# Optimization experiments

Hardware: AMD Instinct MI355X
Metric: run time of the kernel (lower is better)

Reference implementation:

```python
import jax, jax.numpy as jnp
import numpy as np

# FP4 E2M1 value table (codes 0..7 positive, 8..15 negative, sign in MSB)
FP4_VALUES = jnp.array([0.0, 0.5, 1.0, 1.5, 2.0, 3.0, 4.0, 6.0,
                        -0.0, -0.5, -1.0, -1.5, -2.0, -3.0, -4.0, -6.0],
                       dtype=jnp.float32)


def setup_inputs() -> dict:
    key = jax.random.key(0)
    k1, k2, k3, k4 = jax.random.split(key, 4)
    O, I = 4096, 4096
    block = 16
    x = jax.random.normal(k1, (8192, I), dtype=jnp.float32)
    # packed uint4 pairs stored as int32 bytes in [0, 256)
    weight = jax.random.randint(k2, (O, I // 2), 0, 256, dtype=jnp.int32)
    # per-block FP8-style scales (positive)
    weight_scale = jax.random.uniform(k3, (O, I // block), dtype=jnp.float32, minval=0.01, maxval=1.0)
    bias = jax.random.normal(k4, (O,), dtype=jnp.float32)
    return {"x": x, "weight": weight, "weight_scale": weight_scale,
            "bias": bias, "block_size": block}


def _dequant_nvfp4(weight, weight_scale, block_size):
    # unpack two FP4 codes per byte: high nibble is the even (first) element
    hi = (weight >> 4) & 0xF
    lo = weight & 0xF
    O = weight.shape[0]
    codes = jnp.stack([hi, lo], axis=-1).reshape(O, -1)  # [O, I]
    vals = FP4_VALUES[codes]                             # [O, I] f32
    I = vals.shape[1]
    # apply per-block scale
    w = vals.reshape(O, I // block_size, block_size) * weight_scale[:, :, None]
    return w.reshape(O, I)


def reference(x, weight, weight_scale, bias, block_size):
    w = _dequant_nvfp4(weight, weight_scale, block_size)  # [O, I]
    return jnp.einsum('ti,oi->to', x, w) + bias[None, :]
```

## Files before the change

kernel.cpp:

```cpp
#include <hip/hip_runtime.h>
#include <hip/hip_fp16.h>

typedef __attribute__((ext_vector_type(8))) _Float16 f16x8;
typedef __attribute__((ext_vector_type(4))) float f32x4;

#define M_DIM 8192
#define N_DIM 4096
#define K_DIM 4096
#define BM 256
#define BN 256
#define BK 32
#define NT (K_DIM / BK)
#define TILE_F16 ((BM + BN) * BK)

__constant__ float FP4_LUT[16] = {0.f, 0.5f, 1.f, 1.5f, 2.f, 3.f, 4.f, 6.f,
                                  -0.f, -0.5f, -1.f, -1.5f, -2.f, -3.f, -4.f, -6.f};

__device__ inline void glds16(const void* g, void* l) {
    __builtin_amdgcn_global_load_lds(
        (const __attribute__((address_space(1))) void*)g,
        (__attribute__((address_space(3))) void*)l, 16, 0, 0);
}

__global__ __launch_bounds__(256) void cvt_x_kernel(const float* __restrict__ x,
                                                    _Float16* __restrict__ xh) {
    int i = (blockIdx.x * 256 + threadIdx.x) * 8;
    const float4* p = (const float4*)(x + i);
    float4 a = p[0], b = p[1];
    f16x8 h;
    h[0] = (_Float16)a.x; h[1] = (_Float16)a.y;
    h[2] = (_Float16)a.z; h[3] = (_Float16)a.w;
    h[4] = (_Float16)b.x; h[5] = (_Float16)b.y;
    h[6] = (_Float16)b.z; h[7] = (_Float16)b.w;
    *(f16x8*)(xh + i) = h;
}

__global__ __launch_bounds__(256) void dequant_w_kernel(const int* __restrict__ w,
                                                        const float* __restrict__ wsc,
                                                        _Float16* __restrict__ wh) {
    int t = blockIdx.x * 256 + threadIdx.x;
    int4 b4 = ((const int4*)w)[t];
    int o  = t >> 9;
    int j0 = (t & 511) << 2;
    float s = wsc[(o << 8) + (j0 >> 3)];
    f16x8 h;
    int b;
    b = b4.x; h[0] = (_Float16)(FP4_LUT[(b >> 4) & 15] * s); h[1] = (_Float16)(FP4_LUT[b & 15] * s);
    b = b4.y; h[2] = (_Float16)(FP4_LUT[(b >> 4) & 15] * s); h[3] = (_Float16)(FP4_LUT[b & 15] * s);
    b = b4.z; h[4] = (_Float16)(FP4_LUT[(b >> 4) & 15] * s); h[5] = (_Float16)(FP4_LUT[b & 15] * s);
    b = b4.w; h[6] = (_Float16)(FP4_LUT[(b >> 4) & 15] * s); h[7] = (_Float16)(FP4_LUT[b & 15] * s);
    *(f16x8*)(wh + ((long)o << 12) + (j0 << 1)) = h;
}

__global__ __launch_bounds__(512, 2) void gemm_f16_pipe(const _Float16* __restrict__ A,
                                                        const _Float16* __restrict__ B,
                                                        const float* __restrict__ bias,
                                                        float* __restrict__ C) {
    __shared__ _Float16 lds[4 * TILE_F16];

    const int tid  = threadIdx.x;
    const int wid  = tid >> 6;
    const int lane = tid & 63;
    const int fr   = lane & 15;
    const int kg   = lane >> 4;
    const int wm   = wid >> 2;
    const int wn   = wid & 3;

    int bid = blockIdx.x;
    int nb  = (bid & 7) * 64 + (bid >> 3);
    int bm  = nb & 31;
    int bn  = nb >> 5;
    const int brow = bm * BM;
    const int bcol = bn * BN;

    const int s_r = (wid << 4) + (lane >> 2);
    const int s_c = (((lane & 3) ^ ((lane >> 3) & 3)) << 3);

    const _Float16* srcA0 = A + (size_t)(brow +       s_r) * K_DIM + s_c;
    const _Float16* srcA1 = A + (size_t)(brow + 128 + s_r) * K_DIM + s_c;
    const _Float16* srcB0 = B + (size_t)(bcol +       s_r) * K_DIM + s_c;
    const _Float16* srcB1 = B + (size_t)(bcol + 128 + s_r) * K_DIM + s_c;

    const int dA0 = (wid << 9);
    const int dA1 = 4096  + (wid << 9);
    const int dB0 = 8192  + (wid << 9);
    const int dB1 = 12288 + (wid << 9);

    const int swz    = ((kg ^ ((fr >> 1) & 3)) << 3);
    const int a_base = (wm * 128 + fr) * BK + swz;
    const int b_base = BM * BK + (wn * 64 + fr) * BK + swz;

    f32x4 acc[8][4] = {};

#pragma unroll
    for (int p = 0; p < 3; ++p) {
        _Float16* db = lds + p * TILE_F16;
        size_t kk = (size_t)p * BK;
        glds16(srcA0 + kk, db + dA0);
        glds16(srcA1 + kk, db + dA1);
        glds16(srcB0 + kk, db + dB0);
        glds16(srcB1 + kk, db + dB1);
    }

    for (int t = 0; t < NT; ++t) {
        if (t + 2 < NT)      asm volatile("s_waitcnt vmcnt(8)" ::: "memory");
        else if (t + 1 < NT) asm volatile("s_waitcnt vmcnt(4)" ::: "memory");
        else                 asm volatile("s_waitcnt vmcnt(0)" ::: "memory");
        __builtin_amdgcn_s_barrier();
        __builtin_amdgcn_sched_barrier(0);

        if (t + 3 < NT) {
            _Float16* db = lds + ((t + 3) & 3) * TILE_F16;
            size_t kk = (size_t)(t + 3) * BK;
            glds16(srcA0 + kk, db + dA0);
            glds16(srcA1 + kk, db + dA1);
            glds16(srcB0 + kk, db + dB0);
            glds16(srcB1 + kk, db + dB1);
        }

        const _Float16* cb = lds + (t & 3) * TILE_F16;
        f16x8 af[8], bf[4];
#pragma unroll
        for (int m = 0; m < 8; ++m)
            af[m] = *(const f16x8*)(cb + a_base + m * (16 * BK));
#pragma unroll
        for (int n = 0; n < 4; ++n)
            bf[n] = *(const f16x8*)(cb + b_base + n * (16 * BK));

        __builtin_amdgcn_s_setprio(1);
#pragma unroll
        for (int m = 0; m < 8; ++m)
#pragma unroll
            for (int n = 0; n < 4; ++n)
                acc[m][n] = __builtin_amdgcn_mfma_f32_16x16x32_f16(af[m], bf[n], acc[m][n], 0, 0, 0);
        __builtin_amdgcn_s_setprio(0);
    }

#pragma unroll
    for (int m = 0; m < 8; ++m) {
        int row = brow + wm * 128 + m * 16 + kg * 4;
#pragma unroll
        for (int n = 0; n < 4; ++n) {
            int col = bcol + wn * 64 + n * 16 + fr;
            float bv = bias[col];
#pragma unroll
            for (int j = 0; j < 4; ++j)
                C[(size_t)(row + j) * N_DIM + col] = acc[m][n][j] + bv;
        }
    }
}

__global__ __launch_bounds__(256) void fallback_kernel(const float* __restrict__ x,
                                                       const int* __restrict__ w,
                                                       const float* __restrict__ wsc,
                                                       const float* __restrict__ bias,
                                                       float* __restrict__ out) {
    long idx = (long)blockIdx.x * 256 + threadIdx.x;
    int t = (int)(idx >> 12);
    int o = (int)(idx & 4095);
    float acc = 0.f;
    for (int j = 0; j < K_DIM / 2; ++j) {
        int b = w[o * (K_DIM / 2) + j];
        float s = wsc[(o << 8) + (j >> 3)];
        acc += x[(long)t * K_DIM + 2 * j]     * (FP4_LUT[(b >> 4) & 15] * s);
        acc += x[(long)t * K_DIM + 2 * j + 1] * (FP4_LUT[b & 15] * s);
    }
    out[idx] = acc + bias[o];
}

extern "C" void kernel_launch(void* const* d_in, const int* in_sizes, int n_in,
                              void* d_out, int out_size, void* d_ws, size_t ws_size,
                              hipStream_t stream) {
    const float* x    = (const float*)d_in[0];
    const int*   w    = (const int*)d_in[1];
    const float* wsc  = (const float*)d_in[2];
    const float* bias = (const float*)d_in[3];
    float* out = (float*)d_out;

    const size_t xh_bytes = (size_t)M_DIM * K_DIM * 2;
    const size_t wh_bytes = (size_t)N_DIM * K_DIM * 2;

    if (ws_size >= xh_bytes + wh_bytes) {
        _Float16* xh = (_Float16*)d_ws;
        _Float16* wh = (_Float16*)((char*)d_ws + xh_bytes);
        cvt_x_kernel<<<(M_DIM * K_DIM) / (256 * 8), 256, 0, stream>>>(x, xh);
        dequant_w_kernel<<<(N_DIM * (K_DIM / 2)) / (256 * 4), 256, 0, stream>>>(w, wsc, wh);
        gemm_f16_pipe<<<(M_DIM / BM) * (N_DIM / BN), 512, 0, stream>>>(xh, wh, bias, out);
    } else {
        fallback_kernel<<<((long)M_DIM * N_DIM) / 256, 256, 0, stream>>>(x, w, wsc, bias, out);
    }
}
```

Baseline: 309.3 us.

## Restructure GEMM mainloop into 8-phase ping-pong schedule with split LDS loads

Replaces the 4-stage, one-barrier-per-K-step GEMM loop with an explicitly unrolled 8-phase schedule over BK=64. Each phase loads half the A fragments (and the B fragments only every other phase), issues one global-to-LDS stage, and then runs 16 MFMAs between barriers. The goal is to interleave LDS reads, global prefetch and MFMA work more finely and to cut register pressure by keeping only 4 A fragments live. In exchange it adds many more barriers per K block, and it drops the XOR swizzle on LDS reads, which risks bank conflicts.

```diff
diff --git a/kernel.cpp b/kernel.cpp
--- a/kernel.cpp
+++ b/kernel.cpp
@@ -9,9 +9,9 @@
 #define K_DIM 4096
 #define BM 256
 #define BN 256
-#define BK 32
+#define BK 64
 #define NT (K_DIM / BK)
-#define TILE_F16 ((BM + BN) * BK)
+#define ITERS (NT / 2)
 
 __constant__ float FP4_LUT[16] = {0.f, 0.5f, 1.f, 1.5f, 2.f, 3.f, 4.f, 6.f,
                                   -0.f, -0.5f, -1.f, -1.5f, -2.f, -3.f, -4.f, -6.f};
@@ -52,11 +52,54 @@
     *(f16x8*)(wh + ((long)o << 12) + (j0 << 1)) = h;
 }
 
-__global__ __launch_bounds__(512, 2) void gemm_f16_pipe(const _Float16* __restrict__ A,
-                                                        const _Float16* __restrict__ B,
-                                                        const float* __restrict__ bias,
-                                                        float* __restrict__ C) {
-    __shared__ _Float16 lds[4 * TILE_F16];
+
+#define VM8 asm volatile("s_waitcnt vmcnt(8)" ::: "memory")
+#define VM4 asm volatile("s_waitcnt vmcnt(4)" ::: "memory")
+#define VM0 asm volatile("s_waitcnt vmcnt(0)" ::: "memory")
+#define VMX ((void)0)
+
+#define STAGE(OP, SD, KH, KOFF) do {                                           \
+    _Float16* _d = lds + (SD)*32768 + (OP)*16384 + (KH)*8192 + (wid << 9);     \
+    const _Float16* _s = ((OP) ? srcB : srcA) + (KOFF);                        \
+    glds16(_s, _d);                                                            \
+    glds16(_s + (size_t)128 * K_DIM, _d + 4096);                               \
+  } while (0)
+
+#define PHASE(CB, KH, MH, DOB, VMS, ...) do {                                  \
+    const _Float16* _cb = lds + (CB)*32768 + (KH)*8192;                        \
+    if (DOB) {                                                                 \
+      bf[0] = *(const f16x8*)(_cb + b_off);                                    \
+      bf[1] = *(const f16x8*)(_cb + b_off + 512);                              \
+      bf[2] = *(const f16x8*)(_cb + b_off + 1024);                             \
+      bf[3] = *(const f16x8*)(_cb + b_off + 1536);                             \
+    }                                                                          \
+    af[0] = *(const f16x8*)(_cb + a_off + (MH)*2048);                          \
+    af[1] = *(const f16x8*)(_cb + a_off + (MH)*2048 + 512);                    \
+    af[2] = *(const f16x8*)(_cb + a_off + (MH)*2048 + 1024);                   \
+    af[3] = *(const f16x8*)(_cb + a_off + (MH)*2048 + 1536);                   \
+    __VA_ARGS__;                                                               \
+    __builtin_amdgcn_s_barrier();                                              \
+    asm volatile("s_waitcnt lgkmcnt(0)" ::: "memory");                         \
+    __builtin_amdgcn_sched_barrier(0);                                         \
+    __builtin_amdgcn_s_setprio(1);                                             \
+    _Pragma("unroll")                                                          \
+    for (int mf = 0; mf < 4; ++mf) {                                           \
+      _Pragma("unroll")                                                        \
+      for (int nf = 0; nf < 4; ++nf)                                           \
+        acc[(MH)*4 + mf][nf] = __builtin_amdgcn_mfma_f32_16x16x32_f16(         \
+            af[mf], bf[nf], acc[(MH)*4 + mf][nf], 0, 0, 0);                    \
+    }                                                                          \
+    __builtin_amdgcn_s_setprio(0);                                             \
+    __builtin_amdgcn_sched_barrier(0);                                         \
+    VMS;                                                                       \
+    __builtin_amdgcn_s_barrier();                                              \
+  } while (0)
+
+__global__ __launch_bounds__(512, 2) void gemm_f16_8ph(const _Float16* __restrict__ A,
+                                                       const _Float16* __restrict__ B,
+                                                       const float* __restrict__ bias,
+                                                       float* __restrict__ C) {
+    __shared__ _Float16 lds[2 * 32768];
 
     const int tid  = threadIdx.x;
     const int wid  = tid >> 6;
@@ -68,72 +111,48 @@
 
     int bid = blockIdx.x;
     int nb  = (bid & 7) * 64 + (bid >> 3);
-    int bm  = nb & 31;
-    int bn  = nb >> 5;
-    const int brow = bm * BM;
-    const int bcol = bn * BN;
-
-    const int s_r = (wid << 4) + (lane >> 2);
-    const int s_c = (((lane & 3) ^ ((lane >> 3) & 3)) << 3);
-
-    const _Float16* srcA0 = A + (size_t)(brow +       s_r) * K_DIM + s_c;
-    const _Float16* srcA1 = A + (size_t)(brow + 128 + s_r) * K_DIM + s_c;
-    const _Float16* srcB0 = B + (size_t)(bcol +       s_r) * K_DIM + s_c;
-    const _Float16* srcB1 = B + (size_t)(bcol + 128 + s_r) * K_DIM + s_c;
-
-    const int dA0 = (wid << 9);
-    const int dA1 = 4096  + (wid << 9);
-    const int dB0 = 8192  + (wid << 9);
-    const int dB1 = 12288 + (wid << 9);
-
-    const int swz    = ((kg ^ ((fr >> 1) & 3)) << 3);
-    const int a_base = (wm * 128 + fr) * BK + swz;
-    const int b_base = BM * BK + (wn * 64 + fr) * BK + swz;
-
+    const int brow = (nb & 31) * BM;
+    const int bcol = (nb >> 5) * BN;
+
+    const _Float16* srcA = A + (size_t)(brow + (tid >> 2)) * K_DIM + ((tid & 3) << 3);
+    const _Float16* srcB = B + (size_t)(bcol + (tid >> 2)) * K_DIM + ((tid & 3) << 3);
+
+    const int a_off = (wm * 128 + fr) * 32 + (kg << 3);
+    const int b_off = 16384 + (wn * 64 + fr) * 32 + (kg << 3);
+
+    f16x8 af[4], bf[4];
     f32x4 acc[8][4] = {};
 
-#pragma unroll
-    for (int p = 0; p < 3; ++p) {
-        _Float16* db = lds + p * TILE_F16;
-        size_t kk = (size_t)p * BK;
-        glds16(srcA0 + kk, db + dA0);
-        glds16(srcA1 + kk, db + dA1);
-        glds16(srcB0 + kk, db + dB0);
-        glds16(srcB1 + kk, db + dB1);
-    }
-
-    for (int t = 0; t < NT; ++t) {
-        if (t + 2 < NT)      asm volatile("s_waitcnt vmcnt(8)" ::: "memory");
-        else if (t + 1 < NT) asm volatile("s_waitcnt vmcnt(4)" ::: "memory");
-        else                 asm volatile("s_waitcnt vmcnt(0)" ::: "memory");
-        __builtin_amdgcn_s_barrier();
-        __builtin_amdgcn_sched_barrier(0);
-
-        if (t + 3 < NT) {
-            _Float16* db = lds + ((t + 3) & 3) * TILE_F16;
-            size_t kk = (size_t)(t + 3) * BK;
-            glds16(srcA0 + kk, db + dA0);
-            glds16(srcA1 + kk, db + dA1);
-            glds16(srcB0 + kk, db + dB0);
-            glds16(srcB1 + kk, db + dB1);
-        }
-
-        const _Float16* cb = lds + (t & 3) * TILE_F16;
-        f16x8 af[8], bf[4];
-#pragma unroll
-        for (int m = 0; m < 8; ++m)
-            af[m] = *(const f16x8*)(cb + a_base + m * (16 * BK));
-#pragma unroll
-        for (int n = 0; n < 4; ++n)
-            bf[n] = *(const f16x8*)(cb + b_base + n * (16 * BK));
-
-        __builtin_amdgcn_s_setprio(1);
-#pragma unroll
-        for (int m = 0; m < 8; ++m)
-#pragma unroll
-            for (int n = 0; n < 4; ++n)
-                acc[m][n] = __builtin_amdgcn_mfma_f32_16x16x32_f16(af[m], bf[n], acc[m][n], 0, 0, 0);
-        __builtin_amdgcn_s_setprio(0);
+    STAGE(0, 0, 0, 0);
+    STAGE(1, 0, 0, 0);
+    STAGE(0, 0, 1, 32);
+    STAGE(1, 0, 1, 32);
+    STAGE(0, 1, 0, 64);
+    STAGE(1, 1, 0, 64);
+    VM8;
+    __builtin_amdgcn_s_barrier();
+
+    for (int i = 0; i < ITERS - 1; ++i) {
+        const int kb = i << 7;
+        PHASE(0, 0, 0, true,  VMX, STAGE(0, 1, 1, kb + 96));
+        PHASE(0, 0, 1, false, VM8, STAGE(1, 1, 1, kb + 96));
+        PHASE(0, 1, 0, true,  VMX, STAGE(0, 0, 0, kb + 128));
+        PHASE(0, 1, 1, false, VM8, STAGE(1, 0, 0, kb + 128));
+        PHASE(1, 0, 0, true,  VMX, STAGE(0, 0, 1, kb + 160));
+        PHASE(1, 0, 1, false, VM8, STAGE(1, 0, 1, kb + 160));
+        PHASE(1, 1, 0, true,  VMX, STAGE(0, 1, 0, kb + 192));
+        PHASE(1, 1, 1, false, VM8, STAGE(1, 1, 0, kb + 192));
+    }
+    {
+        const int kb = (ITERS - 1) << 7;
+        PHASE(0, 0, 0, true,  VMX, STAGE(0, 1, 1, kb + 96));
+        PHASE(0, 0, 1, false, VM8, STAGE(1, 1, 1, kb + 96));
+        PHASE(0, 1, 0, true,  VMX, VMX);
+        PHASE(0, 1, 1, false, VM4, VMX);
+        PHASE(1, 0, 0, true,  VMX, VMX);
+        PHASE(1, 0, 1, false, VM0, VMX);
+        PHASE(1, 1, 0, true,  VMX, VMX);
+        PHASE(1, 1, 1, false, VMX, VMX);
     }
 
 #pragma unroll
@@ -185,7 +204,7 @@
         _Float16* wh = (_Float16*)((char*)d_ws + xh_bytes);
         cvt_x_kernel<<<(M_DIM * K_DIM) / (256 * 8), 256, 0, stream>>>(x, xh);
         dequant_w_kernel<<<(N_DIM * (K_DIM / 2)) / (256 * 4), 256, 0, stream>>>(w, wsc, wh);
-        gemm_f16_pipe<<<(M_DIM / BM) * (N_DIM / BN), 512, 0, stream>>>(xh, wh, bias, out);
+        gemm_f16_8ph<<<(M_DIM / BM) * (N_DIM / BN), 512, 0, stream>>>(xh, wh, bias, out);
     } else {
         fallback_kernel<<<((long)M_DIM * N_DIM) / 256, 256, 0, stream>>>(x, w, wsc, bias, out);
     }
```

After: 314.4 us. No clear change (+1.7%).
